# Optimization experiments

Hardware: AMD Instinct MI355X
Metric: run time of the kernel (lower is better)

The kernel has to match this reference:

```python
import jax, jax.numpy as jnp
import numpy as np

K, T, D, H = 256, 256, 64, 256
TEMP = 1.0
LOG2 = float(np.log(2.0))


def setup_inputs() -> dict:
    key = jax.random.key(0)
    k1, k2, k3, k4 = jax.random.split(key, 4)
    embeddings_KxtxD = jax.random.normal(k1, (K, T, D), dtype=jnp.float32)
    leaf_counts_Kxt = jax.random.randint(k2, (K, T), 0, 3).astype(jnp.int32)
    W1 = jax.random.normal(k3, (2 * D, H), dtype=jnp.float32) * 0.05
    b1 = jnp.zeros((H,), dtype=jnp.float32)
    W2 = jax.random.normal(k4, (H, D), dtype=jnp.float32) * 0.05
    b2 = jnp.zeros((D,), dtype=jnp.float32)
    return {"N": 256, "leaf_counts_Kxt": leaf_counts_Kxt,
            "embeddings_KxtxD": embeddings_KxtxD, "log": 0,
            "W1": W1, "b1": b1, "W2": W2, "b2": b2}


def _pairwise_dist(emb):  # [K,t,D] -> [K,t,t] Euclidean, no KxtxtxD blowup
    sq = jnp.sum(emb * emb, axis=-1)                       # [K,t]
    gram = jnp.einsum('ktd,ksd->kts', emb, emb)            # [K,t,t]
    d2 = sq[:, :, None] + sq[:, None, :] - 2.0 * gram
    return jnp.sqrt(jnp.maximum(d2, 0.0))


def reference(N, leaf_counts_Kxt, embeddings_KxtxD, log, W1, b1, W2, b2):
    k, t = leaf_counts_Kxt.shape
    dist_Kxtxt = _pairwise_dist(embeddings_KxtxD)
    logw_Kxtxt = -dist_Kxtxt / TEMP
    eye = jnp.eye(t, dtype=bool)
    logw_Kxtxt = jnp.where(eye[None], -jnp.inf, logw_Kxtxt)  # diagonal_scatter(-inf)

    # categorical sample over flattened t*t logits (Gumbel-max)
    skey = jax.random.key(42)
    g = jax.random.gumbel(skey, (k, t * t), dtype=jnp.float32)
    flat_logw = logw_Kxtxt.reshape(k, t * t)
    flat_sample_K = jnp.argmax(flat_logw + g, axis=-1)
    idx1_K = flat_sample_K // t
    idx2_K = flat_sample_K % t

    rows = jnp.arange(k)
    child1_KxD = embeddings_KxtxD[rows, idx1_K]            # gather_K
    child2_KxD = embeddings_KxtxD[rows, idx2_K]

    # merge encoder MLP
    h = jax.nn.relu(jnp.concatenate([child1_KxD, child2_KxD], axis=-1) @ W1 + b1)
    embedding_KxD = h @ W2 + b2

    # sample_branches=False: branch length = distance(child, merged)
    branch1_K = jnp.linalg.norm(child1_KxD - embedding_KxD, axis=-1)
    branch2_K = jnp.linalg.norm(child2_KxD - embedding_KxD, axis=-1)

    log_merge_prob_K = logw_Kxtxt[rows, idx1_K, idx2_K]    # gather_K2
    log_merge_prob_K = log_merge_prob_K + LOG2
    log_merge_prob_K = log_merge_prob_K - jax.scipy.special.logsumexp(
        logw_Kxtxt, axis=(1, 2))
    log_v_plus_K = log_merge_prob_K  # branch priors are 0

    ones_K = jnp.sum((leaf_counts_Kxt == 1).astype(jnp.int32), axis=1)
    ones_K = ones_K - (leaf_counts_Kxt[rows, idx1_K] == 1).astype(jnp.int32)
    ones_K = ones_K - (leaf_counts_Kxt[rows, idx2_K] == 1).astype(jnp.int32)
    v_minus_K = N - ones_K
    log_v_minus_K = jnp.log(v_minus_K.astype(jnp.float32))

    return (idx1_K, idx2_K, branch1_K, branch2_K, embedding_KxD,
            log_v_plus_K, log_v_minus_K)
```

## Files before the change

kernel.cpp:

```cpp
#include <hip/hip_runtime.h>
#include <stdint.h>
#include <math.h>

#define TK 256
#define TT 256
#define DD 64
#define HH 256
#define NTHREADS 1024
#define PADB 72

typedef short bf16x8 __attribute__((ext_vector_type(8)));
typedef float f32x4  __attribute__((ext_vector_type(4)));

__device__ __forceinline__ uint32_t rotl32(uint32_t x, uint32_t d) {
  return (x << d) | (x >> (32u - d));
}
__device__ __forceinline__ uint2 threefry2x32(uint32_t x0, uint32_t x1) {
  const uint32_t ks0 = 0u, ks1 = 42u, ks2 = 0x1BD11BF0u;
  x0 += ks0; x1 += ks1;
#define TFR(r) { x0 += x1; x1 = rotl32(x1, r); x1 ^= x0; }
  TFR(13u) TFR(15u) TFR(26u) TFR(6u)
  x0 += ks1; x1 += ks2 + 1u;
  TFR(17u) TFR(29u) TFR(16u) TFR(24u)
  x0 += ks2; x1 += ks0 + 2u;
  TFR(13u) TFR(15u) TFR(26u) TFR(6u)
  x0 += ks0; x1 += ks1 + 3u;
  TFR(17u) TFR(29u) TFR(16u) TFR(24u)
  x0 += ks1; x1 += ks2 + 4u;
  TFR(13u) TFR(15u) TFR(26u) TFR(6u)
  x0 += ks2; x1 += ks0 + 5u;
#undef TFR
  return make_uint2(x0, x1);
}

__device__ __forceinline__ uint16_t f2bf(float x) {
  uint32_t u = __float_as_uint(x);
  return (uint16_t)((u + 0x7FFFu + ((u >> 16) & 1u)) >> 16);
}

__global__ __launch_bounds__(NTHREADS) void ep_fused(
    const int*   __restrict__ pN,
    const int*   __restrict__ leaf,
    const float* __restrict__ emb,
    const float* __restrict__ W1,
    const float* __restrict__ b1,
    const float* __restrict__ W2,
    const float* __restrict__ b2,
    float*       __restrict__ out)
{
  __shared__ uint16_t s_hi[TT * PADB];
  __shared__ uint16_t s_lo[TT * PADB];
  __shared__ float s_sq[TT];
  __shared__ float s_c1[DD], s_c2[DD];
  __shared__ float s_wss[16], s_wb[16];
  __shared__ int   s_wi[16], s_onesw[16], s_sel[2];
  __shared__ float s_h[HH], s_e[DD];
  __shared__ float s_lse;

  const int k   = blockIdx.x;
  const int tid = threadIdx.x;
  const float* ek = emb + (size_t)k * (TT * DD);

  for (int idx = tid; idx < TT * DD / 4; idx += NTHREADS) {
    float4 v = ((const float4*)ek)[idx];
    int f = idx << 2;
    int r = f >> 6, c = f & 63;
    uint16_t h0 = f2bf(v.x), h1 = f2bf(v.y), h2 = f2bf(v.z), h3 = f2bf(v.w);
    float l0f = v.x - __uint_as_float((uint32_t)h0 << 16);
    float l1f = v.y - __uint_as_float((uint32_t)h1 << 16);
    float l2f = v.z - __uint_as_float((uint32_t)h2 << 16);
    float l3f = v.w - __uint_as_float((uint32_t)h3 << 16);
    uint2 hp = make_uint2((uint32_t)h0 | ((uint32_t)h1 << 16),
                          (uint32_t)h2 | ((uint32_t)h3 << 16));
    uint2 lp = make_uint2((uint32_t)f2bf(l0f) | ((uint32_t)f2bf(l1f) << 16),
                          (uint32_t)f2bf(l2f) | ((uint32_t)f2bf(l3f) << 16));
    *(uint2*)&s_hi[r * PADB + c] = hp;
    *(uint2*)&s_lo[r * PADB + c] = lp;
  }
  if (tid < TT) {
    const float* row = ek + tid * DD;
    float acc = 0.f;
#pragma unroll
    for (int c = 0; c < DD; ++c) acc = fmaf(row[c], row[c], acc);
    s_sq[tid] = acc;
  }
  __syncthreads();

  const int wv = tid >> 6, l = tid & 63;
  const int lm = l & 15, lk = l >> 4;
  const int I0 = wv * 16;

  const char* hib = (const char*)s_hi;
  const char* lob = (const char*)s_lo;
  const int arow = (I0 + lm) * (PADB * 2);
  bf16x8 ah0 = *(const bf16x8*)(hib + arow + lk * 16);
  bf16x8 ah1 = *(const bf16x8*)(hib + arow + 64 + lk * 16);
  bf16x8 al0 = *(const bf16x8*)(lob + arow + lk * 16);
  bf16x8 al1 = *(const bf16x8*)(lob + arow + 64 + lk * 16);

  float sqi_r[4];
#pragma unroll
  for (int r = 0; r < 4; ++r) sqi_r[r] = s_sq[I0 + lk * 4 + r];

  float ss = 0.f, best = -3.402823466e38f;
  int bidx = 0x7fffffff;

  for (int jt = 0; jt < 16; ++jt) {
    const int J0 = jt * 16;
    const int brow = (J0 + lm) * (PADB * 2);
    bf16x8 bh0 = *(const bf16x8*)(hib + brow + lk * 16);
    bf16x8 bh1 = *(const bf16x8*)(hib + brow + 64 + lk * 16);
    bf16x8 bl0 = *(const bf16x8*)(lob + brow + lk * 16);
    bf16x8 bl1 = *(const bf16x8*)(lob + brow + 64 + lk * 16);

    f32x4 acc = {0.f, 0.f, 0.f, 0.f};
    acc = __builtin_amdgcn_mfma_f32_16x16x32_bf16(ah0, bh0, acc, 0, 0, 0);
    acc = __builtin_amdgcn_mfma_f32_16x16x32_bf16(ah0, bl0, acc, 0, 0, 0);
    acc = __builtin_amdgcn_mfma_f32_16x16x32_bf16(al0, bh0, acc, 0, 0, 0);
    acc = __builtin_amdgcn_mfma_f32_16x16x32_bf16(ah1, bh1, acc, 0, 0, 0);
    acc = __builtin_amdgcn_mfma_f32_16x16x32_bf16(ah1, bl1, acc, 0, 0, 0);
    acc = __builtin_amdgcn_mfma_f32_16x16x32_bf16(al1, bh1, acc, 0, 0, 0);

    const int j = J0 + lm;
    const float sqj = s_sq[j];
    const uint32_t pbase = ((uint32_t)k << 16) | (uint32_t)j;

#pragma unroll
    for (int r = 0; r < 4; ++r) {
      const int i = I0 + lk * 4 + r;
      float dsq = sqi_r[r] + sqj - 2.0f * acc[r];
      float lw  = -sqrtf(fmaxf(dsq, 0.f));
      if (i != j) {
        ss += __expf(lw);
        uint2 rr = threefry2x32(0u, pbase + ((uint32_t)i << 8));
        uint32_t bits = rr.x ^ rr.y;
        float f = __uint_as_float((bits >> 9) | 0x3F800000u) - 1.0f;
        float u = fmaxf(f, 1.1754943508222875e-38f);
        float g = -__logf(-__logf(u));
        float sv = lw + g;
        int fi = i * TT + j;
        if (sv > best || (sv == best && fi < bidx)) { best = sv; bidx = fi; }
      }
    }
  }

#pragma unroll
  for (int off = 32; off > 0; off >>= 1) {
    ss += __shfl_xor(ss, off);
    float ob = __shfl_xor(best, off);
    int   oi = __shfl_xor(bidx, off);
    if (ob > best || (ob == best && oi < bidx)) { best = ob; bidx = oi; }
  }
  if (l == 0) { s_wss[wv] = ss; s_wb[wv] = best; s_wi[wv] = bidx; }
  {
    int isone = (tid < TT) ? ((leaf[k * TT + tid] == 1) ? 1 : 0) : 0;
    unsigned long long bal = __ballot(isone);
    if (l == 0) s_onesw[wv] = __popcll(bal);
  }
  __syncthreads();

  if (tid == 0) {
    float tot = 0.f, bb = -3.402823466e38f; int bi = 0x7fffffff;
    for (int w = 0; w < 16; ++w) {
      tot += s_wss[w];
      if (s_wb[w] > bb || (s_wb[w] == bb && s_wi[w] < bi)) { bb = s_wb[w]; bi = s_wi[w]; }
    }
    s_sel[0] = bi >> 8;
    s_sel[1] = bi & 255;
    s_lse    = logf(tot);
  }
  __syncthreads();

  const int i1 = s_sel[0], i2 = s_sel[1];
  if (tid < DD) {
    s_c1[tid] = ek[i1 * DD + tid];
    s_c2[tid] = ek[i2 * DD + tid];
  }
  __syncthreads();

  if (tid < HH) {
    float h0 = 0.f, h1 = 0.f;
#pragma unroll 8
    for (int c = 0; c < DD; ++c) h0 = fmaf(s_c1[c], W1[c * HH + tid], h0);
#pragma unroll 8
    for (int c = 0; c < DD; ++c) h1 = fmaf(s_c2[c], W1[(DD + c) * HH + tid], h1);
    s_h[tid] = fmaxf(h0 + h1 + b1[tid], 0.f);
  }
  __syncthreads();

  if (tid < DD) {
    float acc = 0.f;
#pragma unroll 8
    for (int hh = 0; hh < HH; ++hh) acc = fmaf(s_h[hh], W2[hh * DD + tid], acc);
    float e = acc + b2[tid];
    s_e[tid] = e;
    out[1024 + k * DD + tid] = e;
  }
  __syncthreads();

  if (tid < DD) {
    float dd1 = s_c1[tid] - s_e[tid];
    float dd2 = s_c2[tid] - s_e[tid];
    float q1 = dd1 * dd1, q2 = dd2 * dd2;
#pragma unroll
    for (int off = 32; off > 0; off >>= 1) {
      q1 += __shfl_xor(q1, off);
      q2 += __shfl_xor(q2, off);
    }
    if (tid == 0) {
      out[512 + k] = sqrtf(q1);
      out[768 + k] = sqrtf(q2);
    }
  }

  if (tid == 0) {
    float dot = 0.f;
#pragma unroll
    for (int c = 0; c < DD; ++c) dot = fmaf(s_c1[c], s_c2[c], dot);
    float dsq = s_sq[i1] + s_sq[i2] - 2.0f * dot;
    float lw  = -sqrtf(fmaxf(dsq, 0.f));
    out[0   + k] = (float)i1;
    out[256 + k] = (float)i2;
    out[17408 + k] = lw + 0.69314718055994531f - s_lse;
    int ones = 0;
    for (int w = 0; w < 16; ++w) ones += s_onesw[w];
    ones -= (leaf[k * TT + i1] == 1) ? 1 : 0;
    ones -= (leaf[k * TT + i2] == 1) ? 1 : 0;
    int vminus = pN[0] - ones;
    out[17664 + k] = logf((float)vminus);
  }
}

extern "C" void kernel_launch(void* const* d_in, const int* in_sizes, int n_in,
                              void* d_out, int out_size, void* d_ws, size_t ws_size,
                              hipStream_t stream) {
  const int*   pN   = (const int*)d_in[0];
  const int*   leaf = (const int*)d_in[1];
  const float* emb  = (const float*)d_in[2];
  const float* W1   = (const float*)d_in[4];
  const float* b1   = (const float*)d_in[5];
  const float* W2   = (const float*)d_in[6];
  const float* b2   = (const float*)d_in[7];
  float* out = (float*)d_out;

  ep_fused<<<TK, NTHREADS, 0, stream>>>(pN, leaf, emb, W1, b1, W2, b2, out);
}
```

Baseline: 158.0 us.

## Split each sample's pairwise Gumbel-max across two blocks with atomic combine

Launches two blocks per sample, each covering half of the column tiles in the distance/Gumbel loop. Partial logsumexp sums and packed argmax keys are merged through workspace atomics, and the last-arriving block finishes the MLP and outputs. This aims to spread the hash- and log-heavy loop over more CUs. In exchange, each block redundantly stages the full embedding tile, an extra memset is added, and the float atomic sum makes the result order-dependent.

```diff
diff --git a/kernel.cpp b/kernel.cpp
--- a/kernel.cpp
+++ b/kernel.cpp
@@ -11,6 +11,8 @@
 
 typedef short bf16x8 __attribute__((ext_vector_type(8)));
 typedef float f32x4  __attribute__((ext_vector_type(4)));
+
+struct KWs { unsigned long long packed; float ss; unsigned int arrive; unsigned int pad; };
 
 __device__ __forceinline__ uint32_t rotl32(uint32_t x, uint32_t d) {
   return (x << d) | (x >> (32u - d));
@@ -46,7 +48,8 @@
     const float* __restrict__ b1,
     const float* __restrict__ W2,
     const float* __restrict__ b2,
-    float*       __restrict__ out)
+    float*       __restrict__ out,
+    KWs*         __restrict__ ws)
 {
   __shared__ uint16_t s_hi[TT * PADB];
   __shared__ uint16_t s_lo[TT * PADB];
@@ -56,9 +59,11 @@
   __shared__ int   s_wi[16], s_onesw[16], s_sel[2];
   __shared__ float s_h[HH], s_e[DD];
   __shared__ float s_lse;
-
-  const int k   = blockIdx.x;
-  const int tid = threadIdx.x;
+  __shared__ int   s_exec;
+
+  const int k    = blockIdx.x >> 1;
+  const int half = blockIdx.x & 1;
+  const int tid  = threadIdx.x;
   const float* ek = emb + (size_t)k * (TT * DD);
 
   for (int idx = tid; idx < TT * DD / 4; idx += NTHREADS) {
@@ -105,7 +110,7 @@
   float ss = 0.f, best = -3.402823466e38f;
   int bidx = 0x7fffffff;
 
-  for (int jt = 0; jt < 16; ++jt) {
+  for (int jt = half * 8; jt < half * 8 + 8; ++jt) {
     const int J0 = jt * 16;
     const int brow = (J0 + lm) * (PADB * 2);
     bf16x8 bh0 = *(const bf16x8*)(hib + brow + lk * 16);
@@ -165,11 +170,29 @@
       tot += s_wss[w];
       if (s_wb[w] > bb || (s_wb[w] == bb && s_wi[w] < bi)) { bb = s_wb[w]; bi = s_wi[w]; }
     }
-    s_sel[0] = bi >> 8;
-    s_sel[1] = bi & 255;
-    s_lse    = logf(tot);
-  }
-  __syncthreads();
+    KWs* w = ws + k;
+    uint32_t sb = __float_as_uint(bb);
+    uint32_t mapped = (sb & 0x80000000u) ? ~sb : (sb | 0x80000000u);
+    unsigned long long pk = ((unsigned long long)mapped << 32) |
+                            (unsigned long long)(~(uint32_t)bi);
+    atomicAdd(&w->ss, tot);
+    atomicMax(&w->packed, pk);
+    __threadfence();
+    unsigned int old = atomicAdd(&w->arrive, 1u);
+    if (old == 1u) {
+      float tt = atomicAdd(&w->ss, 0.0f);
+      unsigned long long fp = atomicMax(&w->packed, 0ull);
+      int fbi = (int)(~(uint32_t)(fp & 0xFFFFFFFFull));
+      s_sel[0] = fbi >> 8;
+      s_sel[1] = fbi & 255;
+      s_lse    = logf(tt);
+      s_exec   = 1;
+    } else {
+      s_exec = 0;
+    }
+  }
+  __syncthreads();
+  if (!s_exec) return;
 
   const int i1 = s_sel[0], i2 = s_sel[1];
   if (tid < DD) {
@@ -242,6 +265,8 @@
   const float* W2   = (const float*)d_in[6];
   const float* b2   = (const float*)d_in[7];
   float* out = (float*)d_out;
-
-  ep_fused<<<TK, NTHREADS, 0, stream>>>(pN, leaf, emb, W1, b1, W2, b2, out);
-}
+  KWs*   ws  = (KWs*)d_ws;
+
+  hipMemsetAsync(d_ws, 0, TK * sizeof(KWs), stream);
+  ep_fused<<<TK * 2, NTHREADS, 0, stream>>>(pN, leaf, emb, W1, b1, W2, b2, out, ws);
+}
```

Result: faster. 150.0 us (-5.1%).
